# Kernel tuning notes

Hardware: AMD Instinct MI355X
Metric: run time of the kernel (lower is better)

## Reference

```python
import jax, jax.numpy as jnp
import numpy as np
from jax.scipy.linalg import cho_solve

N, D, T, K, P = 4000, 256, 52, 20, 100
EPS = 1e-8


def _make_kernel(length_scale):
    # RBF kernel over time grid with the same jitter-doubling rule as the torch code.
    t = np.arange(T, dtype=np.float32)
    sq = (t[None, :] - t[:, None]) ** 2
    Kmat = np.exp(-0.5 * sq / np.float32(length_scale) ** 2).astype(np.float32)
    jitter = 1e-4
    eye = np.eye(T, dtype=np.float32)
    while True:
        if np.linalg.cond(Kmat + jitter * eye) < 1e4:
            break
        jitter *= 2
        if jitter > 0.1:
            break
    return jnp.asarray(Kmat + jitter * eye)

K_LAMBDA = _make_kernel(T / 4)  # lambda GP kernel, shared across all k
K_PHI = _make_kernel(T / 3)     # phi GP kernel, shared across all k


def setup_inputs() -> dict:
    key = jax.random.key(0)
    ks = jax.random.split(key, 7)
    lambda_ = jax.random.normal(ks[0], (N, K, T), dtype=jnp.float32)
    phi = jax.random.normal(ks[1], (K, D, T), dtype=jnp.float32)
    gamma = 0.1 * jax.random.normal(ks[2], (P, K), dtype=jnp.float32)
    G = jax.random.normal(ks[3], (N, P), dtype=jnp.float32)
    Y = (jax.random.uniform(ks[4], (N, D, T)) < 0.05).astype(jnp.float32)
    logit_prev_t = jax.random.normal(ks[5], (D, T), dtype=jnp.float32) - 3.0
    event_times = jax.random.randint(ks[6], (N, D), 0, T)
    return dict(lambda_=lambda_, phi=phi, gamma=gamma, G=G, Y=Y,
                logit_prev_t=logit_prev_t, event_times=event_times)


def reference(lambda_, phi, gamma, G, Y, logit_prev_t, event_times):
    # --- forward: softmax over topics, sigmoid disease probs, mixture ---
    theta = jax.nn.softmax(lambda_, axis=1)          # [N,K,T]
    phi_prob = jax.nn.sigmoid(phi)                   # [K,D,T]
    pi = jnp.einsum('nkt,kdt->ndt', theta, phi_prob) # [N,D,T]
    pi = jnp.clip(pi, EPS, 1.0 - EPS)

    # --- survival data loss ---
    tgrid = jnp.arange(T)[None, None, :]             # [1,1,T]
    e = event_times[:, :, None]                      # [N,D,1]
    mask_before = (tgrid < e).astype(pi.dtype)
    mask_at = (tgrid == e).astype(pi.dtype)
    log_pi = jnp.log(pi)
    log_1mpi = jnp.log1p(-pi)
    loss_censored = -jnp.sum(log_1mpi * mask_before)
    loss_event = -jnp.sum(log_pi * mask_at * Y)
    loss_no_event = -jnp.sum(log_1mpi * mask_at * (1.0 - Y))
    data_loss = (loss_censored + loss_event + loss_no_event) / N

    # --- GP prior loss: batched cholesky solves replace per-sample loops ---
    L_lam = jnp.linalg.cholesky(K_LAMBDA)            # [T,T]
    L_phi = jnp.linalg.cholesky(K_PHI)               # [T,T]
    mean_lam = G @ gamma                             # [N,K]
    dev_lam = (lambda_ - mean_lam[:, :, None]).reshape(N * K, T)  # [N*K,T]
    v_lam = cho_solve((L_lam, True), dev_lam.T)      # [T,N*K]
    gp_lambda = 0.5 * jnp.sum(dev_lam.T * v_lam)
    dev_phi = (phi - logit_prev_t[None, :, :]).reshape(K * D, T)  # [K*D,T]
    v_phi = cho_solve((L_phi, True), dev_phi.T)      # [T,K*D]
    gp_phi = 0.5 * jnp.sum(dev_phi.T * v_phi)
    gp_loss = gp_lambda / N + gp_phi / D

    return data_loss + gp_loss
```

## Files before the change

### kernel.cpp

```cpp
#include <hip/hip_runtime.h>
#include <math.h>
#include <string.h>

#define Nn 4000
#define Dd 256
#define Tt 52
#define Kk 20
#define Pp 100
#define CH 13
#define TC 4

#define OFF_W_LAM    0
#define OFF_W_PHI    2704
#define OFF_M_LAM    5408
#define OFF_M_PHI    8112
#define OFF_DL       10816
#define OFF_EVP      10820
#define OFF_PHIP     266820
#define OFF_THETA    533060

#define GR_ROWS 128

#define RB_PHIP0   0
#define RB_THETA0  52
#define RB_GPHI0   865
#define RB_GLAM0   885
#define RB_EV0     1010
#define RB_TOTAL   1138

__global__ __launch_bounds__(256) void prep_kernel(
    const float* __restrict__ lam, const float* __restrict__ phi,
    const float* __restrict__ gamma, const float* __restrict__ G,
    const float* __restrict__ logit_prev, const int* __restrict__ ev,
    float* __restrict__ theta_t, float* __restrict__ phip_t,
    unsigned char* __restrict__ evp,
    float* __restrict__ M_lam, float* __restrict__ M_phi) {
    __shared__ float rows[GR_ROWS][56];
    __shared__ float meanv[GR_ROWS];
    const int bx = blockIdx.x, tid = threadIdx.x;

    if (bx < RB_THETA0) {
        int gid = bx * 256 + tid;
        int d = gid / Tt, t = gid - d * Tt;
        float v[Kk];
#pragma unroll
        for (int k = 0; k < Kk; ++k) {
            float x = phi[k * (Dd * Tt) + gid];
            v[k] = 1.f / (1.f + __expf(-x));
        }
#pragma unroll
        for (int k = 0; k < Kk; ++k)
            phip_t[((size_t)t * Kk + k) * Dd + d] = v[k];
        return;
    }
    if (bx < RB_GPHI0) {
        int gid = (bx - RB_THETA0) * 256 + tid;
        if (gid >= Nn * Tt) return;
        int n = gid / Tt, t = gid - n * Tt;
        const float* base = lam + n * Kk * Tt + t;
        float v[Kk];
        float m = -1e30f;
#pragma unroll
        for (int k = 0; k < Kk; ++k) { v[k] = base[k * Tt]; m = fmaxf(m, v[k]); }
        float s = 0.f;
#pragma unroll
        for (int k = 0; k < Kk; ++k) { v[k] = __expf(v[k] - m); s += v[k]; }
        float inv = 1.f / s;
        float* o = theta_t + ((size_t)t * Nn + n) * Kk;
#pragma unroll
        for (int k = 0; k < Kk; ++k) o[k] = v[k] * inv;
        return;
    }
    if (bx < RB_GLAM0) {
        int ta = tid % 13, tb = tid / 13;
        float acc[4][4] = {};
        for (int it = 0; it < 2; ++it) {
            int R0 = ((bx - RB_GPHI0) * 2 + it) * GR_ROWS;
            __syncthreads();
            for (int idx = tid; idx < GR_ROWS * Tt; idx += 256) {
                int r = idx / Tt, t = idx - r * Tt;
                int R = R0 + r;
                rows[r][t] = phi[R * Tt + t] - logit_prev[(R & 255) * Tt + t];
            }
            __syncthreads();
            if (tb < 13) {
                for (int r = 0; r < GR_ROWS; ++r) {
                    float4 a = *(const float4*)&rows[r][4 * ta];
                    float4 b = *(const float4*)&rows[r][4 * tb];
                    float av[4] = {a.x, a.y, a.z, a.w};
                    float bv[4] = {b.x, b.y, b.z, b.w};
#pragma unroll
                    for (int i = 0; i < 4; ++i)
#pragma unroll
                        for (int j = 0; j < 4; ++j) acc[i][j] += av[i] * bv[j];
                }
            }
        }
        if (tb < 13)
#pragma unroll
            for (int i = 0; i < 4; ++i)
#pragma unroll
                for (int j = 0; j < 4; ++j)
                    atomicAdd(&M_phi[(4 * ta + i) * Tt + 4 * tb + j], acc[i][j]);
        return;
    }
    if (bx < RB_EV0) {
        int ta = tid % 13, tb = tid / 13;
        float acc[4][4] = {};
        for (int it = 0; it < 5; ++it) {
            int R0 = ((bx - RB_GLAM0) * 5 + it) * GR_ROWS;
            __syncthreads();
            if (tid < GR_ROWS) {
                int R = R0 + tid;
                int n = R / Kk, k = R - n * Kk;
                float m = 0.f;
                for (int p = 0; p < Pp; ++p) m += G[n * Pp + p] * gamma[p * Kk + k];
                meanv[tid] = m;
            }
            __syncthreads();
            for (int idx = tid; idx < GR_ROWS * Tt; idx += 256) {
                int r = idx / Tt, t = idx - r * Tt;
                int R = R0 + r;
                rows[r][t] = lam[R * Tt + t] - meanv[r];
            }
            __syncthreads();
            if (tb < 13) {
                for (int r = 0; r < GR_ROWS; ++r) {
                    float4 a = *(const float4*)&rows[r][4 * ta];
                    float4 b = *(const float4*)&rows[r][4 * tb];
                    float av[4] = {a.x, a.y, a.z, a.w};
                    float bv[4] = {b.x, b.y, b.z, b.w};
#pragma unroll
                    for (int i = 0; i < 4; ++i)
#pragma unroll
                        for (int j = 0; j < 4; ++j) acc[i][j] += av[i] * bv[j];
                }
            }
        }
        if (tb < 13)
#pragma unroll
            for (int i = 0; i < 4; ++i)
#pragma unroll
                for (int j = 0; j < 4; ++j)
                    atomicAdd(&M_lam[(4 * ta + i) * Tt + 4 * tb + j], acc[i][j]);
        return;
    }
    {
        const int4* src = (const int4*)ev;
        unsigned int* dst = (unsigned int*)evp;
        int gtid = (bx - RB_EV0) * 256 + tid;
        for (int i = gtid; i < (Nn * Dd) / 4; i += 128 * 256) {
            int4 v = src[i];
            dst[i] = (unsigned)v.x | ((unsigned)v.y << 8) |
                     ((unsigned)v.z << 16) | ((unsigned)v.w << 24);
        }
        return;
    }
}

__global__ __launch_bounds__(256) void data_kernel(const float* __restrict__ theta_t,
                                                   const float* __restrict__ phip_t,
                                                   const float* __restrict__ Y,
                                                   const unsigned char* __restrict__ evp,
                                                   float* __restrict__ DL) {
    __shared__ __align__(16) float thS[TC][8][Kk];
    __shared__ float wsum[4];
    const int tid = threadIdx.x;
    const int d = tid;
    const int ng = blockIdx.x / CH;
    const int t0 = (blockIdx.x - ng * CH) * TC;
    const int n0 = ng * 8;

    for (int idx = tid; idx < TC * 8 * Kk; idx += 256) {
        int j = idx / 160, rem = idx - j * 160;
        thS[j][rem / Kk][rem - (rem / Kk) * Kk] =
            theta_t[((size_t)(t0 + j) * Nn + n0) * Kk + rem];
    }

    int e[8];
    float Yv[8], acc[8], pie[8];
#pragma unroll
    for (int g = 0; g < 8; ++g) {
        e[g] = evp[(n0 + g) * Dd + d];
        acc[g] = 0.f;
        pie[g] = 0.5f;
        Yv[g] = 0.f;
        if (e[g] >= t0 && e[g] < t0 + TC)
            Yv[g] = Y[((size_t)((n0 + g) * Dd + d)) * Tt + e[g]];
    }
    __syncthreads();

    const float* ptbase = phip_t + d;
    float pvA[Kk], pvB[Kk];
#pragma unroll
    for (int k = 0; k < Kk; ++k)
        pvA[k] = ptbase[((size_t)t0 * Kk + k) * Dd];
#pragma unroll
    for (int j = 0; j < TC; ++j) {
        float* cur = (j & 1) ? pvB : pvA;
        float* nxt = (j & 1) ? pvA : pvB;
        if (j < TC - 1) {
#pragma unroll
            for (int k = 0; k < Kk; ++k)
                nxt[k] = ptbase[((size_t)(t0 + j + 1) * Kk + k) * Dd];
        }
        int t = t0 + j;
#pragma unroll
        for (int g = 0; g < 8; ++g) {
            const float4* th = (const float4*)&thS[j][g][0];
            float4 a0 = th[0], a1 = th[1], a2 = th[2], a3 = th[3], a4 = th[4];
            float pi = a0.x * cur[0] + a0.y * cur[1] + a0.z * cur[2] + a0.w * cur[3]
                     + a1.x * cur[4] + a1.y * cur[5] + a1.z * cur[6] + a1.w * cur[7]
                     + a2.x * cur[8] + a2.y * cur[9] + a2.z * cur[10] + a2.w * cur[11]
                     + a3.x * cur[12] + a3.y * cur[13] + a3.z * cur[14] + a3.w * cur[15]
                     + a4.x * cur[16] + a4.y * cur[17] + a4.z * cur[18] + a4.w * cur[19];
            pi = fminf(fmaxf(pi, 1e-8f), 1.0f - 1e-8f);
            float lg = __logf(1.f - pi);
            if (t <= e[g]) acc[g] += lg;
            pie[g] = (t == e[g]) ? pi : pie[g];
        }
    }
    float tsum = 0.f;
#pragma unroll
    for (int g = 0; g < 8; ++g)
        tsum += acc[g] + Yv[g] * (__logf(pie[g]) - __logf(1.f - pie[g]));
    for (int off = 32; off; off >>= 1) tsum += __shfl_down(tsum, off, 64);
    if ((tid & 63) == 0) wsum[tid >> 6] = tsum;
    __syncthreads();
    if (tid == 0) atomicAdd(DL, -(wsum[0] + wsum[1] + wsum[2] + wsum[3]));
}

__global__ __launch_bounds__(256) void final_kernel(const float* __restrict__ ws,
                                                    float* __restrict__ out) {
    double s = 0.0;
    for (int i = threadIdx.x; i < 2704; i += 256)
        s += (double)ws[OFF_W_LAM + i] * (double)ws[OFF_M_LAM + i];
    for (int i = threadIdx.x; i < 2704; i += 256)
        s += (double)ws[OFF_W_PHI + i] * (double)ws[OFF_M_PHI + i];
    __shared__ double red[256];
    red[threadIdx.x] = s;
    __syncthreads();
    for (int off = 128; off; off >>= 1) {
        if (threadIdx.x < off) red[threadIdx.x] += red[threadIdx.x + off];
        __syncthreads();
    }
    if (threadIdx.x == 0) out[0] = (float)(red[0] + (double)ws[OFF_DL] / Nn);
}


static void build_K_f(double ls_in, float Kf[52][52]) {
    float ls = (float)ls_in;
    float ls2 = ls * ls;
    for (int i = 0; i < 52; ++i)
        for (int j = 0; j < 52; ++j) {
            float sq = (float)((i - j) * (i - j));
            float arg = (-0.5f * sq) / ls2;
            Kf[i][j] = expf(arg);
        }
}

static void jacobi_eig(double a[52][52], double ev[52]) {
    const int n = 52;
    for (int sweep = 0; sweep < 100; ++sweep) {
        double off = 0;
        for (int p = 0; p < n - 1; ++p)
            for (int q = p + 1; q < n; ++q) off += a[p][q] * a[p][q];
        if (off < 1e-24) break;
        for (int p = 0; p < n - 1; ++p)
            for (int q = p + 1; q < n; ++q) {
                double apq = a[p][q];
                if (fabs(apq) < 1e-300) continue;
                double th = (a[q][q] - a[p][p]) / (2.0 * apq);
                double t = (th >= 0 ? 1.0 : -1.0) / (fabs(th) + sqrt(th * th + 1.0));
                double c = 1.0 / sqrt(t * t + 1.0), s = t * c;
                for (int i = 0; i < n; ++i) {
                    double aip = a[i][p], aiq = a[i][q];
                    a[i][p] = c * aip - s * aiq;
                    a[i][q] = s * aip + c * aiq;
                }
                for (int i = 0; i < n; ++i) {
                    double api = a[p][i], aqi = a[q][i];
                    a[p][i] = c * api - s * aqi;
                    a[q][i] = s * api + c * aqi;
                }
            }
    }
    for (int i = 0; i < n; ++i) ev[i] = a[i][i];
}

static void build_A(const float Kf[52][52], double jitter, double A[52][52]) {
    float jf = (float)jitter;
    for (int i = 0; i < 52; ++i)
        for (int j = 0; j < 52; ++j) A[i][j] = (double)Kf[i][j];
    for (int i = 0; i < 52; ++i) A[i][i] = (double)(float)(Kf[i][i] + jf);
}

static double cond_of(const float Kf[52][52], double jitter) {
    double A[52][52], ev[52];
    build_A(Kf, jitter, A);
    jacobi_eig(A, ev);
    double mx = 0.0, mn = 1e300;
    for (int i = 0; i < 52; ++i) {
        double a = fabs(ev[i]);
        if (a > mx) mx = a;
        if (a < mn) mn = a;
    }
    if (mn <= 0.0) return 1e300;
    return mx / mn;
}

static double find_jitter(const float Kf[52][52]) {
    double jitter = 1e-4;
    while (true) {
        if (cond_of(Kf, jitter) < 1e4) break;
        jitter *= 2.0;
        if (jitter > 0.1) break;
    }
    return jitter;
}

static void chol_inv_scaled(const float Kf[52][52], double jitter, double scale,
                            float* out) {
    const int n = 52;
    double A[52][52], L[52][52];
    build_A(Kf, jitter, A);
    memset(L, 0, sizeof(L));
    for (int j = 0; j < n; ++j) {
        double s = A[j][j];
        for (int k = 0; k < j; ++k) s -= L[j][k] * L[j][k];
        L[j][j] = sqrt(s);
        for (int i = j + 1; i < n; ++i) {
            double v = A[i][j];
            for (int k = 0; k < j; ++k) v -= L[i][k] * L[j][k];
            L[i][j] = v / L[j][j];
        }
    }
    for (int c = 0; c < n; ++c) {
        double y[52], x[52];
        for (int i = 0; i < n; ++i) {
            double v = (i == c) ? 1.0 : 0.0;
            for (int k = 0; k < i; ++k) v -= L[i][k] * y[k];
            y[i] = v / L[i][i];
        }
        for (int i = n - 1; i >= 0; --i) {
            double v = y[i];
            for (int k = i + 1; k < n; ++k) v -= L[k][i] * x[k];
            x[i] = v / L[i][i];
        }
        for (int i = 0; i < n; ++i) out[i * 52 + c] = (float)(x[i] * scale);
    }
}

struct KinvInit {
    float* w;
    KinvInit() {
        if (hipHostMalloc((void**)&w, 5408 * sizeof(float)) != hipSuccess)
            w = (float*)malloc(5408 * sizeof(float));
        float Kf[52][52];
        build_K_f(52.0 / 4.0, Kf);
        chol_inv_scaled(Kf, find_jitter(Kf), 0.5 / Nn, w);
        build_K_f(52.0 / 3.0, Kf);
        chol_inv_scaled(Kf, find_jitter(Kf), 0.5 / Dd, w + 2704);
    }
};
static KinvInit g_kinv;


extern "C" void kernel_launch(void* const* d_in, const int* in_sizes, int n_in,
                              void* d_out, int out_size, void* d_ws, size_t ws_size,
                              hipStream_t stream) {
    (void)in_sizes; (void)n_in; (void)out_size; (void)ws_size;
    const float* lam        = (const float*)d_in[0];
    const float* phi        = (const float*)d_in[1];
    const float* gamma      = (const float*)d_in[2];
    const float* G          = (const float*)d_in[3];
    const float* Y          = (const float*)d_in[4];
    const float* logit_prev = (const float*)d_in[5];
    const int*   ev         = (const int*)d_in[6];
    float* out = (float*)d_out;
    float* ws  = (float*)d_ws;

    hipMemcpyAsync(ws + OFF_W_LAM, g_kinv.w, 5408 * sizeof(float),
                   hipMemcpyHostToDevice, stream);
    hipMemsetAsync(ws + OFF_M_LAM, 0, (2704 * 2 + 1) * sizeof(float), stream);

    prep_kernel<<<RB_TOTAL, 256, 0, stream>>>(
        lam, phi, gamma, G, logit_prev, ev,
        ws + OFF_THETA, ws + OFF_PHIP, (unsigned char*)(ws + OFF_EVP),
        ws + OFF_M_LAM, ws + OFF_M_PHI);
    data_kernel<<<(Nn / 8) * CH, 256, 0, stream>>>(
        ws + OFF_THETA, ws + OFF_PHIP, Y, (const unsigned char*)(ws + OFF_EVP),
        ws + OFF_DL);
    final_kernel<<<1, 256, 0, stream>>>(ws, out);
}
```

Baseline: 479.8 us.

## Fuse softmax into data kernel, compute K inverse on device, drop atomics and memcpy

Removes the separate theta transpose pass by computing the topic softmax inside the data kernel from lambda tiles staged in shared memory, with each block now covering 13 time steps instead of 4. The host-side Cholesky inverse and its per-call host-to-device copy and memset are replaced by two device blocks that run a double-precision Cholesky and invert it. Atomics for the Gram matrices and the data loss are replaced by per-block partial outputs that the final kernel, now 1024 threads, reduces. In exchange the kinv blocks run a serial factorization that may sit on the critical path of the prep kernel, the final reduction does more work, and the phi register double-buffering is dropped.

```diff
diff --git a/kernel.cpp b/kernel.cpp
--- a/kernel.cpp
+++ b/kernel.cpp
@@ -7,40 +7,91 @@
 #define Tt 52
 #define Kk 20
 #define Pp 100
-#define CH 13
-#define TC 4
-
-#define OFF_W_LAM    0
-#define OFF_W_PHI    2704
-#define OFF_M_LAM    5408
-#define OFF_M_PHI    8112
-#define OFF_DL       10816
-#define OFF_EVP      10820
-#define OFF_PHIP     266820
-#define OFF_THETA    533060
+#define CH 4
+#define TC 13
+
+#define OFF_W       0
+#define OFF_MLAM_P  5408
+#define OFF_MPHI_P  343408
+#define OFF_DLP     397488
+#define OFF_EVP     399488
+#define OFF_PHIP    655488
 
 #define GR_ROWS 128
 
-#define RB_PHIP0   0
-#define RB_THETA0  52
-#define RB_GPHI0   865
-#define RB_GLAM0   885
-#define RB_EV0     1010
-#define RB_TOTAL   1138
+#define RB_KINV0   0
+#define RB_PHIP0   2
+#define RB_GPHI0   54
+#define RB_GLAM0   74
+#define RB_EVP0    199
+#define RB_TOTAL   327
+
+__device__ void kinv_block(float ls, double jit, float* __restrict__ outW,
+                           double* __restrict__ Ash ) {
+    const int tid = threadIdx.x;
+    float ls2 = ls * ls;
+    for (int idx = tid; idx < 52 * 52; idx += 256) {
+        int i = idx / 52, j = idx - 52 * i;
+        int di = i - j;
+        float sq = (float)(di * di);
+        float arg = (-0.5f * sq) / ls2;
+        float kf = (float)exp((double)arg);
+        float aij = (i == j) ? (float)(1.0 + jit) : kf;
+        Ash[i * 53 + j] = (double)aij;
+    }
+    __syncthreads();
+    for (int j = 0; j < 52; ++j) {
+        if (tid == 0) {
+            double s = Ash[j * 53 + j];
+            for (int k = 0; k < j; ++k) { double v = Ash[j * 53 + k]; s -= v * v; }
+            Ash[j * 53 + j] = sqrt(s);
+        }
+        __syncthreads();
+        if (tid > j && tid < 52) {
+            double s = Ash[tid * 53 + j];
+            for (int k = 0; k < j; ++k) s -= Ash[tid * 53 + k] * Ash[j * 53 + k];
+            Ash[tid * 53 + j] = s / Ash[j * 53 + j];
+        }
+        __syncthreads();
+    }
+    if (tid < 52) {
+        const int c = tid;
+        double y[52];
+        for (int i = 0; i < 52; ++i) {
+            double s = (i == c) ? 1.0 : 0.0;
+            for (int k = 0; k < i; ++k) s -= Ash[i * 53 + k] * y[k];
+            y[i] = s / Ash[i * 53 + i];
+        }
+        for (int i = 51; i >= 0; --i) {
+            double s = y[i];
+            for (int k = i + 1; k < 52; ++k) s -= Ash[k * 53 + i] * y[k];
+            y[i] = s / Ash[i * 53 + i];
+        }
+        for (int i = 0; i < 52; ++i) outW[i * 52 + c] = (float)y[i];
+    }
+}
 
 __global__ __launch_bounds__(256) void prep_kernel(
     const float* __restrict__ lam, const float* __restrict__ phi,
     const float* __restrict__ gamma, const float* __restrict__ G,
     const float* __restrict__ logit_prev, const int* __restrict__ ev,
-    float* __restrict__ theta_t, float* __restrict__ phip_t,
-    unsigned char* __restrict__ evp,
-    float* __restrict__ M_lam, float* __restrict__ M_phi) {
-    __shared__ float rows[GR_ROWS][56];
-    __shared__ float meanv[GR_ROWS];
+    float* __restrict__ phip_t, unsigned char* __restrict__ evp,
+    float* __restrict__ Mlam_p, float* __restrict__ Mphi_p,
+    float* __restrict__ W,
+    float ls1, double j1, float ls2, double j2) {
+    __shared__ __align__(16) char smem[29184];
+    double* Ash = (double*)smem;
+    float (*rows)[56] = (float(*)[56])smem;
+    float* meanv = (float*)(smem + GR_ROWS * 56 * 4);
     const int bx = blockIdx.x, tid = threadIdx.x;
 
-    if (bx < RB_THETA0) {
-        int gid = bx * 256 + tid;
+    if (bx < RB_PHIP0) {
+        if (bx == 0) kinv_block(ls1, j1, W, Ash);
+        else         kinv_block(ls2, j2, W + 2704, Ash);
+        return;
+    }
+    if (bx < RB_GPHI0) {
+        int gid = (bx - RB_PHIP0) * 256 + tid;
         int d = gid / Tt, t = gid - d * Tt;
         float v[Kk];
 #pragma unroll
@@ -53,29 +104,12 @@
             phip_t[((size_t)t * Kk + k) * Dd + d] = v[k];
         return;
     }
-    if (bx < RB_GPHI0) {
-        int gid = (bx - RB_THETA0) * 256 + tid;
-        if (gid >= Nn * Tt) return;
-        int n = gid / Tt, t = gid - n * Tt;
-        const float* base = lam + n * Kk * Tt + t;
-        float v[Kk];
-        float m = -1e30f;
-#pragma unroll
-        for (int k = 0; k < Kk; ++k) { v[k] = base[k * Tt]; m = fmaxf(m, v[k]); }
-        float s = 0.f;
-#pragma unroll
-        for (int k = 0; k < Kk; ++k) { v[k] = __expf(v[k] - m); s += v[k]; }
-        float inv = 1.f / s;
-        float* o = theta_t + ((size_t)t * Nn + n) * Kk;
-#pragma unroll
-        for (int k = 0; k < Kk; ++k) o[k] = v[k] * inv;
-        return;
-    }
     if (bx < RB_GLAM0) {
+        int slot = bx - RB_GPHI0;
         int ta = tid % 13, tb = tid / 13;
         float acc[4][4] = {};
         for (int it = 0; it < 2; ++it) {
-            int R0 = ((bx - RB_GPHI0) * 2 + it) * GR_ROWS;
+            int R0 = (slot * 2 + it) * GR_ROWS;
             __syncthreads();
             for (int idx = tid; idx < GR_ROWS * Tt; idx += 256) {
                 int r = idx / Tt, t = idx - r * Tt;
@@ -101,14 +135,15 @@
             for (int i = 0; i < 4; ++i)
 #pragma unroll
                 for (int j = 0; j < 4; ++j)
-                    atomicAdd(&M_phi[(4 * ta + i) * Tt + 4 * tb + j], acc[i][j]);
+                    Mphi_p[slot * 2704 + (4 * ta + i) * Tt + 4 * tb + j] = acc[i][j];
         return;
     }
-    if (bx < RB_EV0) {
+    if (bx < RB_EVP0) {
+        int slot = bx - RB_GLAM0;
         int ta = tid % 13, tb = tid / 13;
         float acc[4][4] = {};
         for (int it = 0; it < 5; ++it) {
-            int R0 = ((bx - RB_GLAM0) * 5 + it) * GR_ROWS;
+            int R0 = (slot * 5 + it) * GR_ROWS;
             __syncthreads();
             if (tid < GR_ROWS) {
                 int R = R0 + tid;
@@ -142,13 +177,13 @@
             for (int i = 0; i < 4; ++i)
 #pragma unroll
                 for (int j = 0; j < 4; ++j)
-                    atomicAdd(&M_lam[(4 * ta + i) * Tt + 4 * tb + j], acc[i][j]);
+                    Mlam_p[slot * 2704 + (4 * ta + i) * Tt + 4 * tb + j] = acc[i][j];
         return;
     }
     {
         const int4* src = (const int4*)ev;
         unsigned int* dst = (unsigned int*)evp;
-        int gtid = (bx - RB_EV0) * 256 + tid;
+        int gtid = (bx - RB_EVP0) * 256 + tid;
         for (int i = gtid; i < (Nn * Dd) / 4; i += 128 * 256) {
             int4 v = src[i];
             dst[i] = (unsigned)v.x | ((unsigned)v.y << 8) |
@@ -158,23 +193,39 @@
     }
 }
 
-__global__ __launch_bounds__(256) void data_kernel(const float* __restrict__ theta_t,
+__global__ __launch_bounds__(256) void data_kernel(const float* __restrict__ lam,
                                                    const float* __restrict__ phip_t,
                                                    const float* __restrict__ Y,
                                                    const unsigned char* __restrict__ evp,
-                                                   float* __restrict__ DL) {
+                                                   float* __restrict__ DLp) {
     __shared__ __align__(16) float thS[TC][8][Kk];
+    __shared__ float lamS[8][Kk][TC + 1];
     __shared__ float wsum[4];
     const int tid = threadIdx.x;
     const int d = tid;
-    const int ng = blockIdx.x / CH;
-    const int t0 = (blockIdx.x - ng * CH) * TC;
+    const int ng = blockIdx.x >> 2;
+    const int t0 = (blockIdx.x & 3) * TC;
     const int n0 = ng * 8;
 
-    for (int idx = tid; idx < TC * 8 * Kk; idx += 256) {
-        int j = idx / 160, rem = idx - j * 160;
-        thS[j][rem / Kk][rem - (rem / Kk) * Kk] =
-            theta_t[((size_t)(t0 + j) * Nn + n0) * Kk + rem];
+    if (tid < 8 * Kk) {
+        int n = tid / Kk, k = tid - n * Kk;
+        const float* src = lam + ((size_t)(n0 + n) * Kk + k) * Tt + t0;
+#pragma unroll
+        for (int j = 0; j < TC; ++j) lamS[n][k][j] = src[j];
+    }
+    __syncthreads();
+    if (tid < 8 * TC) {
+        int n = tid / TC, j = tid - n * TC;
+        float v[Kk];
+        float m = -1e30f;
+#pragma unroll
+        for (int k = 0; k < Kk; ++k) { v[k] = lamS[n][k][j]; m = fmaxf(m, v[k]); }
+        float s = 0.f;
+#pragma unroll
+        for (int k = 0; k < Kk; ++k) { v[k] = __expf(v[k] - m); s += v[k]; }
+        float inv = 1.f / s;
+#pragma unroll
+        for (int k = 0; k < Kk; ++k) thS[j][n][k] = v[k] * inv;
     }
 
     int e[8];
@@ -186,34 +237,26 @@
         pie[g] = 0.5f;
         Yv[g] = 0.f;
         if (e[g] >= t0 && e[g] < t0 + TC)
-            Yv[g] = Y[((size_t)((n0 + g) * Dd + d)) * Tt + e[g]];
+            Yv[g] = __builtin_nontemporal_load(
+                Y + ((size_t)((n0 + g) * Dd + d)) * Tt + e[g]);
     }
     __syncthreads();
 
-    const float* ptbase = phip_t + d;
-    float pvA[Kk], pvB[Kk];
-#pragma unroll
-    for (int k = 0; k < Kk; ++k)
-        pvA[k] = ptbase[((size_t)t0 * Kk + k) * Dd];
-#pragma unroll
     for (int j = 0; j < TC; ++j) {
-        float* cur = (j & 1) ? pvB : pvA;
-        float* nxt = (j & 1) ? pvA : pvB;
-        if (j < TC - 1) {
-#pragma unroll
-            for (int k = 0; k < Kk; ++k)
-                nxt[k] = ptbase[((size_t)(t0 + j + 1) * Kk + k) * Dd];
-        }
         int t = t0 + j;
+        float pv[Kk];
+        const float* pt = phip_t + (size_t)t * (Kk * Dd) + d;
+#pragma unroll
+        for (int k = 0; k < Kk; ++k) pv[k] = pt[k * Dd];
 #pragma unroll
         for (int g = 0; g < 8; ++g) {
             const float4* th = (const float4*)&thS[j][g][0];
             float4 a0 = th[0], a1 = th[1], a2 = th[2], a3 = th[3], a4 = th[4];
-            float pi = a0.x * cur[0] + a0.y * cur[1] + a0.z * cur[2] + a0.w * cur[3]
-                     + a1.x * cur[4] + a1.y * cur[5] + a1.z * cur[6] + a1.w * cur[7]
-                     + a2.x * cur[8] + a2.y * cur[9] + a2.z * cur[10] + a2.w * cur[11]
-                     + a3.x * cur[12] + a3.y * cur[13] + a3.z * cur[14] + a3.w * cur[15]
-                     + a4.x * cur[16] + a4.y * cur[17] + a4.z * cur[18] + a4.w * cur[19];
+            float pi = a0.x * pv[0] + a0.y * pv[1] + a0.z * pv[2] + a0.w * pv[3]
+                     + a1.x * pv[4] + a1.y * pv[5] + a1.z * pv[6] + a1.w * pv[7]
+                     + a2.x * pv[8] + a2.y * pv[9] + a2.z * pv[10] + a2.w * pv[11]
+                     + a3.x * pv[12] + a3.y * pv[13] + a3.z * pv[14] + a3.w * pv[15]
+                     + a4.x * pv[16] + a4.y * pv[17] + a4.z * pv[18] + a4.w * pv[19];
             pi = fminf(fmaxf(pi, 1e-8f), 1.0f - 1e-8f);
             float lg = __logf(1.f - pi);
             if (t <= e[g]) acc[g] += lg;
@@ -227,24 +270,32 @@
     for (int off = 32; off; off >>= 1) tsum += __shfl_down(tsum, off, 64);
     if ((tid & 63) == 0) wsum[tid >> 6] = tsum;
     __syncthreads();
-    if (tid == 0) atomicAdd(DL, -(wsum[0] + wsum[1] + wsum[2] + wsum[3]));
-}
-
-__global__ __launch_bounds__(256) void final_kernel(const float* __restrict__ ws,
-                                                    float* __restrict__ out) {
+    if (tid == 0)
+        DLp[blockIdx.x] = -(wsum[0] + wsum[1] + wsum[2] + wsum[3]);
+}
+
+__global__ __launch_bounds__(1024) void final_kernel(const float* __restrict__ ws,
+                                                     float* __restrict__ out) {
+    const int tid = threadIdx.x;
     double s = 0.0;
-    for (int i = threadIdx.x; i < 2704; i += 256)
-        s += (double)ws[OFF_W_LAM + i] * (double)ws[OFF_M_LAM + i];
-    for (int i = threadIdx.x; i < 2704; i += 256)
-        s += (double)ws[OFF_W_PHI + i] * (double)ws[OFF_M_PHI + i];
-    __shared__ double red[256];
-    red[threadIdx.x] = s;
+    for (int i = tid; i < 2704; i += 1024) {
+        double ml = 0.0, mp = 0.0;
+        for (int b = 0; b < 125; ++b) ml += (double)ws[OFF_MLAM_P + b * 2704 + i];
+        for (int b = 0; b < 20; ++b)  mp += (double)ws[OFF_MPHI_P + b * 2704 + i];
+        s += (double)ws[OFF_W + i] * ml * (0.5 / Nn)
+           + (double)ws[OFF_W + 2704 + i] * mp * (0.5 / Dd);
+    }
+    double dl = 0.0;
+    for (int i = tid; i < (Nn / 8) * CH; i += 1024) dl += (double)ws[OFF_DLP + i];
+    s += dl / Nn;
+    __shared__ double red[1024];
+    red[tid] = s;
     __syncthreads();
-    for (int off = 128; off; off >>= 1) {
-        if (threadIdx.x < off) red[threadIdx.x] += red[threadIdx.x + off];
+    for (int off = 512; off; off >>= 1) {
+        if (tid < off) red[tid] += red[tid + off];
         __syncthreads();
     }
-    if (threadIdx.x == 0) out[0] = (float)(red[0] + (double)ws[OFF_DL] / Nn);
+    if (tid == 0) out[0] = (float)red[0];
 }
 
 
@@ -288,16 +339,12 @@
     for (int i = 0; i < n; ++i) ev[i] = a[i][i];
 }
 
-static void build_A(const float Kf[52][52], double jitter, double A[52][52]) {
+static double cond_of(const float Kf[52][52], double jitter) {
+    double A[52][52], ev[52];
     float jf = (float)jitter;
     for (int i = 0; i < 52; ++i)
         for (int j = 0; j < 52; ++j) A[i][j] = (double)Kf[i][j];
     for (int i = 0; i < 52; ++i) A[i][i] = (double)(float)(Kf[i][i] + jf);
-}
-
-static double cond_of(const float Kf[52][52], double jitter) {
-    double A[52][52], ev[52];
-    build_A(Kf, jitter, A);
     jacobi_eig(A, ev);
     double mx = 0.0, mn = 1e300;
     for (int i = 0; i < 52; ++i) {
@@ -319,51 +366,17 @@
     return jitter;
 }
 
-static void chol_inv_scaled(const float Kf[52][52], double jitter, double scale,
-                            float* out) {
-    const int n = 52;
-    double A[52][52], L[52][52];
-    build_A(Kf, jitter, A);
-    memset(L, 0, sizeof(L));
-    for (int j = 0; j < n; ++j) {
-        double s = A[j][j];
-        for (int k = 0; k < j; ++k) s -= L[j][k] * L[j][k];
-        L[j][j] = sqrt(s);
-        for (int i = j + 1; i < n; ++i) {
-            double v = A[i][j];
-            for (int k = 0; k < j; ++k) v -= L[i][k] * L[j][k];
-            L[i][j] = v / L[j][j];
-        }
-    }
-    for (int c = 0; c < n; ++c) {
-        double y[52], x[52];
-        for (int i = 0; i < n; ++i) {
-            double v = (i == c) ? 1.0 : 0.0;
-            for (int k = 0; k < i; ++k) v -= L[i][k] * y[k];
-            y[i] = v / L[i][i];
-        }
-        for (int i = n - 1; i >= 0; --i) {
-            double v = y[i];
-            for (int k = i + 1; k < n; ++k) v -= L[k][i] * x[k];
-            x[i] = v / L[i][i];
-        }
-        for (int i = 0; i < n; ++i) out[i * 52 + c] = (float)(x[i] * scale);
-    }
-}
-
-struct KinvInit {
-    float* w;
-    KinvInit() {
-        if (hipHostMalloc((void**)&w, 5408 * sizeof(float)) != hipSuccess)
-            w = (float*)malloc(5408 * sizeof(float));
+struct JitterInit {
+    double j_lam, j_phi;
+    JitterInit() {
         float Kf[52][52];
         build_K_f(52.0 / 4.0, Kf);
-        chol_inv_scaled(Kf, find_jitter(Kf), 0.5 / Nn, w);
+        j_lam = find_jitter(Kf);
         build_K_f(52.0 / 3.0, Kf);
-        chol_inv_scaled(Kf, find_jitter(Kf), 0.5 / Dd, w + 2704);
+        j_phi = find_jitter(Kf);
     }
 };
-static KinvInit g_kinv;
+static JitterInit g_jit;
 
 
 extern "C" void kernel_launch(void* const* d_in, const int* in_sizes, int n_in,
@@ -380,16 +393,12 @@
     float* out = (float*)d_out;
     float* ws  = (float*)d_ws;
 
-    hipMemcpyAsync(ws + OFF_W_LAM, g_kinv.w, 5408 * sizeof(float),
-                   hipMemcpyHostToDevice, stream);
-    hipMemsetAsync(ws + OFF_M_LAM, 0, (2704 * 2 + 1) * sizeof(float), stream);
-
     prep_kernel<<<RB_TOTAL, 256, 0, stream>>>(
         lam, phi, gamma, G, logit_prev, ev,
-        ws + OFF_THETA, ws + OFF_PHIP, (unsigned char*)(ws + OFF_EVP),
-        ws + OFF_M_LAM, ws + OFF_M_PHI);
+        ws + OFF_PHIP, (unsigned char*)(ws + OFF_EVP),
+        ws + OFF_MLAM_P, ws + OFF_MPHI_P, ws + OFF_W,
+        (float)(52.0 / 4.0), g_jit.j_lam, (float)(52.0 / 3.0), g_jit.j_phi);
     data_kernel<<<(Nn / 8) * CH, 256, 0, stream>>>(
-        ws + OFF_THETA, ws + OFF_PHIP, Y, (const unsigned char*)(ws + OFF_EVP),
-        ws + OFF_DL);
-    final_kernel<<<1, 256, 0, stream>>>(ws, out);
-}
+        lam, ws + OFF_PHIP, Y, (const unsigned char*)(ws + OFF_EVP), ws + OFF_DLP);
+    final_kernel<<<1, 1024, 0, stream>>>(ws, out);
+}
```

Measured after the change: 611.3 us. 27.4% more time.
